# Optimization experiments

Hardware: AMD Instinct MI355X
Metric: run time of the kernel (lower is better)

Reference implementation:

```python
import jax, jax.numpy as jnp
import numpy as np

N, T, D, H = 4, 2048, 1024, 16
DK = D // H

def setup_inputs() -> dict:
    key = jax.random.key(0)
    k1, k2, k3 = jax.random.split(key, 3)
    z = jax.random.normal(k1, (N, T, D), dtype=jnp.float32)
    Wqkv = jax.random.normal(k2, (D, 3 * D), dtype=jnp.float32) * 0.01
    Wout = jax.random.normal(k3, (D, D), dtype=jnp.float32) * 0.01
    return {"z": z, "Wqkv": Wqkv, "Wout": Wout}

def reference(z, Wqkv, Wout):
    n, t, d = z.shape
    scale = DK ** -0.5
    qkv = z @ Wqkv  # [N,T,3D]
    q, k, v = jnp.split(qkv, 3, axis=-1)
    # [N,T,D] -> [N,H,T,dk]
    q = q.reshape(n, t, H, DK).transpose(0, 2, 1, 3)
    k = k.reshape(n, t, H, DK).transpose(0, 2, 1, 3)
    v = v.reshape(n, t, H, DK).transpose(0, 2, 1, 3)
    attn = jnp.einsum('nhqd,nhkd->nhqk', q, k) * scale
    causal = jnp.tril(jnp.ones((t, t), dtype=bool))
    attn = jnp.where(causal, attn, -jnp.inf)
    attn = jax.nn.softmax(attn, axis=-1)
    out = jnp.einsum('nhqk,nhkd->nhqd', attn, v)  # [N,H,T,dk]
    out = out.transpose(0, 2, 1, 3).reshape(n, t, d)
    return out @ Wout
```

## Files before the change

kernel.cpp:

```cpp
#include <hip/hip_runtime.h>
#include <hip/hip_bf16.h>

typedef __bf16 bf16;
typedef __bf16 bf16x8 __attribute__((ext_vector_type(8)));
typedef float f32x4 __attribute__((ext_vector_type(4)));

#define N_B 4
#define T_S 2048
#define D_M 1024
#define H_N 16
#define D_K 64
#define D3 3072
#define NEG_BIG (-1e30f)
#define QSCALE 0.18033688011112042f

#if __has_builtin(__builtin_amdgcn_exp2f)
#define EXP2(x) __builtin_amdgcn_exp2f(x)
#else
#define EXP2(x) exp2f(x)
#endif

__device__ __forceinline__ void gload_lds16(const bf16* g, bf16* l) {
    __builtin_amdgcn_global_load_lds((const __attribute__((address_space(1))) void*)g,
                                     (__attribute__((address_space(3))) void*)l, 16, 0, 0);
}

__device__ __forceinline__ bool probe_fp32(const void* p) {
    const unsigned int* w = (const unsigned int*)p;
    int weird = 0;
#pragma unroll
    for (int i = 0; i < 16; ++i) {
        unsigned int v = w[i];
        unsigned int e = (v >> 7) & 0xFFu;
        if ((v & 0xFFFFu) != 0u && (e < 100u || e > 140u)) weird++;
    }
    return weird >= 4;
}

__global__ __launch_bounds__(256) void prep(const void* __restrict__ z, bf16* __restrict__ zb,
                                            const void* __restrict__ Wqkv, bf16* __restrict__ WqkvT,
                                            const void* __restrict__ Wout, bf16* __restrict__ WoutT) {
    __shared__ bf16 tile[32][33];
    const int b = blockIdx.x;
    const int t = threadIdx.x;

    if (b < 4096) {
        const int i = (b * 256 + t) * 8;
        if (probe_fp32(z)) {
            const float* zf = (const float*)z;
            float4 u0 = *(const float4*)(zf + i);
            float4 u1 = *(const float4*)(zf + i + 4);
            union { uint4 q; bf16 h[8]; } pk;
            pk.h[0] = (bf16)u0.x; pk.h[1] = (bf16)u0.y;
            pk.h[2] = (bf16)u0.z; pk.h[3] = (bf16)u0.w;
            pk.h[4] = (bf16)u1.x; pk.h[5] = (bf16)u1.y;
            pk.h[6] = (bf16)u1.z; pk.h[7] = (bf16)u1.w;
            *(uint4*)(zb + i) = pk.q;
        } else {
            *(uint4*)(zb + i) = ((const uint4*)z)[b * 256 + t];
        }
        return;
    }

    const void* in; bf16* out; int R, C, c0, r0;
    if (b < 7168) {
        int idx = b - 4096;
        in = Wqkv; out = WqkvT; R = 1024; C = 3072;
        c0 = (idx % 96) * 32; r0 = (idx / 96) * 32;
    } else {
        int idx = b - 7168;
        in = Wout; out = WoutT; R = 1024; C = 1024;
        c0 = (idx & 31) * 32; r0 = (idx >> 5) * 32;
    }
    const int tx = t & 31, ty = t >> 5;
    if (probe_fp32(in)) {
        const float* inf_ = (const float*)in;
        for (int i = 0; i < 4; ++i)
            tile[ty + i * 8][tx] = (bf16)inf_[(size_t)(r0 + ty + i * 8) * C + c0 + tx];
    } else {
        const bf16* inb = (const bf16*)in;
        for (int i = 0; i < 4; ++i)
            tile[ty + i * 8][tx] = inb[(size_t)(r0 + ty + i * 8) * C + c0 + tx];
    }
    __syncthreads();
    for (int i = 0; i < 4; ++i)
        out[(size_t)(c0 + ty + i * 8) * R + r0 + tx] = tile[tx][ty + i * 8];
}

__global__ __launch_bounds__(256) void gemm128(const bf16* __restrict__ A,
                                               const bf16* __restrict__ Bt,
                                               void* __restrict__ C,
                                               bf16* __restrict__ Kf,
                                               bf16* __restrict__ Vf,
                                               int M, int N, int K,
                                               int modeC) {
    __shared__ bf16 As[128 * 64];
    __shared__ bf16 Bs[128 * 64];
    const int t = threadIdx.x;
    const int m0 = blockIdx.y * 128, n0 = blockIdx.x * 128;
    const int w = t >> 6, lane = t & 63, quad = lane >> 4, l15 = lane & 15;
    const int wr = (w >> 1) * 64, wc = (w & 1) * 64;

    f32x4 acc[4][4];
    const f32x4 zero4 = {0.f, 0.f, 0.f, 0.f};
    for (int i = 0; i < 4; ++i)
        for (int j = 0; j < 4; ++j) acc[i][j] = zero4;

    int srow[4], sseg[4];
#pragma unroll
    for (int i = 0; i < 4; ++i) {
        int c = i * 256 + t;
        srow[i] = c >> 3;
        sseg[i] = ((c & 7) * 8) ^ ((srow[i] & 7) * 8);
    }
    const int xorL = (l15 & 7) * 8;

    for (int k0 = 0; k0 < K; k0 += 64) {
        __syncthreads();
#pragma unroll
        for (int i = 0; i < 4; ++i) {
            gload_lds16(A + (size_t)(m0 + srow[i]) * K + k0 + sseg[i],
                        As + (size_t)(i * 256 + w * 64) * 8);
            gload_lds16(Bt + (size_t)(n0 + srow[i]) * K + k0 + sseg[i],
                        Bs + (size_t)(i * 256 + w * 64) * 8);
        }
        __syncthreads();

#pragma unroll
        for (int kk = 0; kk < 2; ++kk) {
            const int colOff = (kk * 32 + quad * 8) ^ xorL;
            bf16x8 af[4], bfv[4];
#pragma unroll
            for (int i = 0; i < 4; ++i)
                af[i] = *(const bf16x8*)(As + (wr + i * 16 + l15) * 64 + colOff);
#pragma unroll
            for (int j = 0; j < 4; ++j)
                bfv[j] = *(const bf16x8*)(Bs + (wc + j * 16 + l15) * 64 + colOff);
#pragma unroll
            for (int i = 0; i < 4; ++i)
#pragma unroll
                for (int j = 0; j < 4; ++j)
                    acc[i][j] = __builtin_amdgcn_mfma_f32_16x16x32_bf16(af[i], bfv[j], acc[i][j], 0, 0, 0);
        }
    }

    if (modeC == 1) {
        float* Cf = (float*)C;
        for (int i = 0; i < 4; ++i)
            for (int fc = 0; fc < 4; ++fc)
                for (int r = 0; r < 4; ++r)
                    Cf[(size_t)(m0 + wr + i * 16 + quad * 4 + r) * N
                       + (n0 + wc + fc * 16 + l15)] = acc[i][fc][r];
    } else if (n0 < 1024) {
        bf16* q = (bf16*)C;
        for (int i = 0; i < 4; ++i)
            for (int fc = 0; fc < 4; ++fc)
                for (int r = 0; r < 4; ++r)
                    q[(size_t)(m0 + wr + i * 16 + quad * 4 + r) * 1024
                      + (n0 + wc + fc * 16 + l15)] = (bf16)(acc[i][fc][r] * QSCALE);
    } else if (n0 < 2048) {
        for (int i = 0; i < 4; ++i) {
            int rowb = m0 + wr + i * 16 + quad * 4;
            int nb = rowb >> 11, tt = rowb & 2047;
            int kt = tt >> 6, f = (tt >> 4) & 3, l15k = tt & 15;
            for (int fc = 0; fc < 4; ++fc) {
                int col = n0 + wc + fc * 16 + l15 - 1024;
                int h = col >> 6, dk = col & 63;
                int ks = dk >> 5, qdk = (dk >> 3) & 3, j = dk & 7;
                size_t base = ((size_t)((nb * 16 + h) * 32 + kt) * 8 + ks * 4 + f) * 512 + j;
                for (int r = 0; r < 4; ++r)
                    Kf[base + (qdk * 16 + l15k + r) * 8] = (bf16)acc[i][fc][r];
            }
        }
    } else {
        for (int i = 0; i < 4; ++i) {
            int rowb = m0 + wr + i * 16 + quad * 4;
            int nb = rowb >> 11, tt = rowb & 2047;
            int kt = tt >> 6, ks = (tt >> 5) & 1, qdv = (tt >> 3) & 3, j0 = tt & 7;
            for (int fc = 0; fc < 4; ++fc) {
                int col = n0 + wc + fc * 16 + l15 - 2048;
                int h = col >> 6, dl = col & 63;
                int fv = dl >> 4, l15v = dl & 15;
                union { ushort4 u; bf16 hh[4]; } pk;
                for (int r = 0; r < 4; ++r) pk.hh[r] = (bf16)acc[i][fc][r];
                *(ushort4*)(Vf + ((size_t)((nb * 16 + h) * 32 + kt) * 8 + ks * 4 + fv) * 512
                            + (qdv * 16 + l15v) * 8 + j0) = pk.u;
            }
        }
    }
}

#define LDP 72
__global__ __launch_bounds__(256, 2) void attn_fused(const bf16* __restrict__ q,
                                                     const bf16* __restrict__ Kf,
                                                     const bf16* __restrict__ Vf,
                                                     bf16* __restrict__ attn_out) {
    __shared__ bf16 Pl[4 * 32 * LDP];

    const int b = blockIdx.x;
    const int head = b & 63;
    const int qp = b >> 6;
    const int n = head >> 4, h = head & 15;
    const int t = threadIdx.x;
    const int w = t >> 6, lane = t & 63, qd = lane >> 4, l15 = lane & 15;
    const int r = (w + qp + head) & 3;
    const int qt = (r < 2) ? qp : (31 - qp);
    const int q0w = qt * 64 + (r & 1) * 32;
    const size_t rowBase = (size_t)n * T_S;
    const bf16* KfH = Kf + (size_t)head * 32 * 4096;
    const bf16* VfH = Vf + (size_t)head * 32 * 4096;
    bf16* Plw = Pl + w * 32 * LDP;

    bf16x8 bQ[2][2];
#pragma unroll
    for (int qh = 0; qh < 2; ++qh)
#pragma unroll
        for (int ks = 0; ks < 2; ++ks)
            bQ[qh][ks] = *(const bf16x8*)(q + (rowBase + q0w + qh * 16 + l15) * 1024
                                          + h * 64 + ks * 32 + qd * 8);

    float l_lane[2] = {0.f, 0.f};
    f32x4 oacc[2][4];
    const f32x4 zero4 = {0.f, 0.f, 0.f, 0.f};
#pragma unroll
    for (int qh = 0; qh < 2; ++qh)
#pragma unroll
        for (int fd = 0; fd < 4; ++fd) oacc[qh][fd] = zero4;

    const int ktmax = (q0w + 31) >> 6;

    bf16x8 aK[2][4];
#pragma unroll
    for (int fr = 0; fr < 8; ++fr)
        aK[fr >> 2][fr & 3] = *(const bf16x8*)(KfH + fr * 512 + lane * 8);

    for (int kt = 0; kt <= ktmax; ++kt) {
        const int k0r = kt * 64;
        const bf16* VfT = VfH + (size_t)kt * 4096;

        bf16x8 aV[2][4];
#pragma unroll
        for (int fr = 0; fr < 8; ++fr)
            aV[fr >> 2][fr & 3] = *(const bf16x8*)(VfT + fr * 512 + lane * 8);

        f32x4 sacc[2][4];
#pragma unroll
        for (int qh = 0; qh < 2; ++qh)
#pragma unroll
            for (int fc = 0; fc < 4; ++fc) sacc[qh][fc] = zero4;
#pragma unroll
        for (int ks = 0; ks < 2; ++ks)
#pragma unroll
            for (int fc = 0; fc < 4; ++fc) {
                sacc[0][fc] = __builtin_amdgcn_mfma_f32_16x16x32_bf16(aK[ks][fc], bQ[0][ks], sacc[0][fc], 0, 0, 0);
                sacc[1][fc] = __builtin_amdgcn_mfma_f32_16x16x32_bf16(aK[ks][fc], bQ[1][ks], sacc[1][fc], 0, 0, 0);
            }

        if (kt < ktmax) {
            const bf16* KfN = KfH + (size_t)(kt + 1) * 4096;
#pragma unroll
            for (int fr = 0; fr < 8; ++fr)
                aK[fr >> 2][fr & 3] = *(const bf16x8*)(KfN + fr * 512 + lane * 8);
        }

        if (k0r + 63 > q0w) {
#pragma unroll
            for (int qh = 0; qh < 2; ++qh) {
                const int qq = q0w + qh * 16 + l15;
#pragma unroll
                for (int fc = 0; fc < 4; ++fc)
#pragma unroll
                    for (int rr = 0; rr < 4; ++rr)
                        if (k0r + fc * 16 + qd * 4 + rr > qq) sacc[qh][fc][rr] = NEG_BIG;
            }
        }

#pragma unroll
        for (int qh = 0; qh < 2; ++qh) {
            float rs = 0.f;
#pragma unroll
            for (int fc = 0; fc < 4; ++fc) {
                union { ushort4 u; bf16 hh[4]; } pk;
#pragma unroll
                for (int rr = 0; rr < 4; ++rr) {
                    float p = EXP2(sacc[qh][fc][rr]);
                    rs += p;
                    pk.hh[rr] = (bf16)p;
                }
                *(ushort4*)(Plw + (qh * 16 + l15) * LDP + fc * 16 + qd * 4) = pk.u;
            }
            l_lane[qh] += rs;
        }

#pragma unroll
        for (int ks = 0; ks < 2; ++ks) {
            bf16x8 bP0 = *(const bf16x8*)(Plw + l15 * LDP + ks * 32 + qd * 8);
            bf16x8 bP1 = *(const bf16x8*)(Plw + (16 + l15) * LDP + ks * 32 + qd * 8);
#pragma unroll
            for (int fd = 0; fd < 4; ++fd) {
                oacc[0][fd] = __builtin_amdgcn_mfma_f32_16x16x32_bf16(aV[ks][fd], bP0, oacc[0][fd], 0, 0, 0);
                oacc[1][fd] = __builtin_amdgcn_mfma_f32_16x16x32_bf16(aV[ks][fd], bP1, oacc[1][fd], 0, 0, 0);
            }
        }
    }

#pragma unroll
    for (int qh = 0; qh < 2; ++qh) {
        float l = l_lane[qh];
        l += __shfl_xor(l, 16, 64);
        l += __shfl_xor(l, 32, 64);
        float inv = 1.f / l;
#pragma unroll
        for (int fd = 0; fd < 4; ++fd) {
            union { ushort4 u; bf16 hh[4]; } pk;
#pragma unroll
            for (int rr = 0; rr < 4; ++rr) pk.hh[rr] = (bf16)(oacc[qh][fd][rr] * inv);
            *(ushort4*)(attn_out + (rowBase + q0w + qh * 16 + l15) * D_M
                        + h * D_K + fd * 16 + qd * 4) = pk.u;
        }
    }
}

extern "C" void kernel_launch(void* const* d_in, const int* in_sizes, int n_in,
                              void* d_out, int out_size, void* d_ws, size_t ws_size,
                              hipStream_t stream) {
    const void* z    = d_in[0];
    const void* Wqkv = d_in[1];
    const void* Wout = d_in[2];

    char* ws = (char*)d_ws;
    bf16* q     = (bf16*)(ws + 256);
    bf16* attn  = (bf16*)(ws + 256 + 16777216);
    bf16* zb    = attn;
    bf16* WqkvT = (bf16*)(ws + 256 + 2 * 16777216);
    bf16* WoutT = (bf16*)(ws + 256 + 2 * 16777216 + 6291456);

    bf16* Kf = (bf16*)d_out;
    bf16* Vf = Kf + 8388608;

    prep<<<dim3(8192), 256, 0, stream>>>(z, zb, Wqkv, WqkvT, Wout, WoutT);

    gemm128<<<dim3(D3 / 128, (N_B * T_S) / 128), 256, 0, stream>>>(
        zb, WqkvT, q, Kf, Vf, N_B * T_S, D3, D_M, 2);

    attn_fused<<<dim3(64 * 16), 256, 0, stream>>>(q, Kf, Vf, attn);

    gemm128<<<dim3(D_M / 128, (N_B * T_S) / 128), 256, 0, stream>>>(
        attn, WoutT, d_out, Kf, Vf, N_B * T_S, D_M, D_M, 1);
}
```

Baseline: 238.1 us.

## Triple-buffer GEMM LDS loads with 256x128 tiles and 512-thread blocks

Replaces the 128x128 single-buffered GEMM with a 256x128 tile computed by 8 waves. Global-to-LDS loads are staged in a three-slot ring so the next two K-steps prefetch while the current one runs MFMAs. Explicit vmcnt waits and a single barrier per step replace the two syncthreads per iteration, and s_setprio raises priority around the MFMA burst. This uses far more LDS (144KB), which limits occupancy, and it halves the block count for the smaller output projection GEMM.

```diff
diff --git a/kernel.cpp b/kernel.cpp
--- a/kernel.cpp
+++ b/kernel.cpp
@@ -87,61 +87,97 @@
         out[(size_t)(c0 + ty + i * 8) * R + r0 + tx] = tile[tx][ty + i * 8];
 }
 
-__global__ __launch_bounds__(256) void gemm128(const bf16* __restrict__ A,
-                                               const bf16* __restrict__ Bt,
-                                               void* __restrict__ C,
-                                               bf16* __restrict__ Kf,
-                                               bf16* __restrict__ Vf,
-                                               int M, int N, int K,
-                                               int modeC) {
-    __shared__ bf16 As[128 * 64];
-    __shared__ bf16 Bs[128 * 64];
+__global__ __launch_bounds__(512, 2) void gemm256(const bf16* __restrict__ A,
+                                                  const bf16* __restrict__ Bt,
+                                                  void* __restrict__ C,
+                                                  bf16* __restrict__ Kf,
+                                                  bf16* __restrict__ Vf,
+                                                  int M, int N, int K,
+                                                  int modeC) {
+    __shared__ bf16 As[3][256 * 64];
+    __shared__ bf16 Bs[3][128 * 64];
     const int t = threadIdx.x;
-    const int m0 = blockIdx.y * 128, n0 = blockIdx.x * 128;
+    const int m0 = blockIdx.y * 256, n0 = blockIdx.x * 128;
     const int w = t >> 6, lane = t & 63, quad = lane >> 4, l15 = lane & 15;
     const int wr = (w >> 1) * 64, wc = (w & 1) * 64;
+    const int sr = t >> 3;
+    const int sg = ((t & 7) ^ (sr & 7)) * 8;
+    const int xorL = (l15 & 7) * 8;
+
+    const bf16* a0 = A + (size_t)(m0 + sr) * K + sg;
+    const bf16* a1 = A + (size_t)(m0 + 64 + sr) * K + sg;
+    const bf16* a2 = A + (size_t)(m0 + 128 + sr) * K + sg;
+    const bf16* a3 = A + (size_t)(m0 + 192 + sr) * K + sg;
+    const bf16* b0 = Bt + (size_t)(n0 + sr) * K + sg;
+    const bf16* b1 = Bt + (size_t)(n0 + 64 + sr) * K + sg;
+    const int ldsOff = w * 512;
 
     f32x4 acc[4][4];
     const f32x4 zero4 = {0.f, 0.f, 0.f, 0.f};
+#pragma unroll
     for (int i = 0; i < 4; ++i)
+#pragma unroll
         for (int j = 0; j < 4; ++j) acc[i][j] = zero4;
 
-    int srow[4], sseg[4];
-#pragma unroll
-    for (int i = 0; i < 4; ++i) {
-        int c = i * 256 + t;
-        srow[i] = c >> 3;
-        sseg[i] = ((c & 7) * 8) ^ ((srow[i] & 7) * 8);
-    }
-    const int xorL = (l15 & 7) * 8;
-
-    for (int k0 = 0; k0 < K; k0 += 64) {
-        __syncthreads();
-#pragma unroll
-        for (int i = 0; i < 4; ++i) {
-            gload_lds16(A + (size_t)(m0 + srow[i]) * K + k0 + sseg[i],
-                        As + (size_t)(i * 256 + w * 64) * 8);
-            gload_lds16(Bt + (size_t)(n0 + srow[i]) * K + k0 + sseg[i],
-                        Bs + (size_t)(i * 256 + w * 64) * 8);
-        }
-        __syncthreads();
-
+    const int nt = K >> 6;
+
+    gload_lds16(a0, &As[0][0 * 4096 + ldsOff]);
+    gload_lds16(a1, &As[0][1 * 4096 + ldsOff]);
+    gload_lds16(a2, &As[0][2 * 4096 + ldsOff]);
+    gload_lds16(a3, &As[0][3 * 4096 + ldsOff]);
+    gload_lds16(b0, &Bs[0][0 * 4096 + ldsOff]);
+    gload_lds16(b1, &Bs[0][1 * 4096 + ldsOff]);
+    gload_lds16(a0 + 64, &As[1][0 * 4096 + ldsOff]);
+    gload_lds16(a1 + 64, &As[1][1 * 4096 + ldsOff]);
+    gload_lds16(a2 + 64, &As[1][2 * 4096 + ldsOff]);
+    gload_lds16(a3 + 64, &As[1][3 * 4096 + ldsOff]);
+    gload_lds16(b0 + 64, &Bs[1][0 * 4096 + ldsOff]);
+    gload_lds16(b1 + 64, &Bs[1][1 * 4096 + ldsOff]);
+
+    int cur = 0;
+    for (int tt = 0; tt < nt; ++tt) {
+        asm volatile("s_waitcnt lgkmcnt(0)" ::: "memory");
+        if (tt + 1 < nt) {
+            asm volatile("s_waitcnt vmcnt(6)" ::: "memory");
+        } else {
+            asm volatile("s_waitcnt vmcnt(0)" ::: "memory");
+        }
+        __builtin_amdgcn_sched_barrier(0);
+        __builtin_amdgcn_s_barrier();
+        __builtin_amdgcn_sched_barrier(0);
+
+        if (tt + 2 < nt) {
+            int pf = cur + 2; if (pf >= 3) pf -= 3;
+            const int kpf = (tt + 2) << 6;
+            gload_lds16(a0 + kpf, &As[pf][0 * 4096 + ldsOff]);
+            gload_lds16(a1 + kpf, &As[pf][1 * 4096 + ldsOff]);
+            gload_lds16(a2 + kpf, &As[pf][2 * 4096 + ldsOff]);
+            gload_lds16(a3 + kpf, &As[pf][3 * 4096 + ldsOff]);
+            gload_lds16(b0 + kpf, &Bs[pf][0 * 4096 + ldsOff]);
+            gload_lds16(b1 + kpf, &Bs[pf][1 * 4096 + ldsOff]);
+        }
+
+        const bf16* Ac = As[cur];
+        const bf16* Bc = Bs[cur];
 #pragma unroll
         for (int kk = 0; kk < 2; ++kk) {
             const int colOff = (kk * 32 + quad * 8) ^ xorL;
             bf16x8 af[4], bfv[4];
 #pragma unroll
             for (int i = 0; i < 4; ++i)
-                af[i] = *(const bf16x8*)(As + (wr + i * 16 + l15) * 64 + colOff);
+                af[i] = *(const bf16x8*)(Ac + (wr + i * 16 + l15) * 64 + colOff);
 #pragma unroll
             for (int j = 0; j < 4; ++j)
-                bfv[j] = *(const bf16x8*)(Bs + (wc + j * 16 + l15) * 64 + colOff);
+                bfv[j] = *(const bf16x8*)(Bc + (wc + j * 16 + l15) * 64 + colOff);
+            __builtin_amdgcn_s_setprio(1);
 #pragma unroll
             for (int i = 0; i < 4; ++i)
 #pragma unroll
                 for (int j = 0; j < 4; ++j)
                     acc[i][j] = __builtin_amdgcn_mfma_f32_16x16x32_bf16(af[i], bfv[j], acc[i][j], 0, 0, 0);
-        }
+            __builtin_amdgcn_s_setprio(0);
+        }
+        cur = cur + 1; if (cur == 3) cur = 0;
     }
 
     if (modeC == 1) {
@@ -340,11 +376,11 @@
 
     prep<<<dim3(8192), 256, 0, stream>>>(z, zb, Wqkv, WqkvT, Wout, WoutT);
 
-    gemm128<<<dim3(D3 / 128, (N_B * T_S) / 128), 256, 0, stream>>>(
+    gemm256<<<dim3(D3 / 128, (N_B * T_S) / 256), 512, 0, stream>>>(
         zb, WqkvT, q, Kf, Vf, N_B * T_S, D3, D_M, 2);
 
     attn_fused<<<dim3(64 * 16), 256, 0, stream>>>(q, Kf, Vf, attn);
 
-    gemm128<<<dim3(D_M / 128, (N_B * T_S) / 128), 256, 0, stream>>>(
+    gemm256<<<dim3(D_M / 128, (N_B * T_S) / 256), 512, 0, stream>>>(
         attn, WoutT, d_out, Kf, Vf, N_B * T_S, D_M, D_M, 1);
 }
```

Result: slower. 243.5 us (+2.3%).
